# Kernel optimization log

Measured on AMD Instinct MI355X. Metric: run time of the kernel, lower is better.

## Reference

```python
import jax, jax.numpy as jnp
import numpy as np

B, N, DIM = 4, 2048, 1024
HEADS, DIM_HEAD = 16, 64
INNER = HEADS * DIM_HEAD  # 1024
SCALE = DIM_HEAD ** -0.5


def setup_inputs() -> dict:
    key = jax.random.key(0)
    k_x, k_qkv, k_out, k_b = jax.random.split(key, 4)
    x = jax.random.normal(k_x, (B, N, DIM), dtype=jnp.float32)
    # nn.Linear weights, stored transposed for x @ W convenience
    w_qkv = jax.random.normal(k_qkv, (DIM, 3 * INNER), dtype=jnp.float32) * (DIM ** -0.5)
    w_out = jax.random.normal(k_out, (INNER, DIM), dtype=jnp.float32) * (INNER ** -0.5)
    b_out = jax.random.normal(k_b, (DIM,), dtype=jnp.float32) * 0.01
    return {"x": x, "w_qkv": w_qkv, "w_out": w_out, "b_out": b_out}


def _split_heads(t):
    # 'b n (h d) -> (b h) n d'
    b, n, _ = t.shape
    return t.reshape(b, n, HEADS, DIM_HEAD).transpose(0, 2, 1, 3).reshape(b * HEADS, n, DIM_HEAD)


def reference(x, w_qkv, w_out, b_out):
    b, n, _ = x.shape
    qkv = x @ w_qkv  # [b, n, 3*inner]
    q, k, v = jnp.split(qkv, 3, axis=-1)
    q = q * SCALE
    q, k, v = map(_split_heads, (q, k, v))  # [(b h), n, d]
    sim = jnp.einsum('bid,bjd->bij', q, k)  # [(b h), n, n]
    a = jax.nn.softmax(sim, axis=-1)
    out = jnp.einsum('bij,bjd->bid', a, v)  # [(b h), n, d]
    # '(b h) n d -> b n (h d)'
    out = out.reshape(b, HEADS, n, DIM_HEAD).transpose(0, 2, 1, 3).reshape(b, n, INNER)
    return out @ w_out + b_out  # dropout p=0.0 is identity
```

## Files before the change

### kernel.cpp

```cpp
#include <hip/hip_runtime.h>
#include <stdint.h>


typedef uint16_t u16;
typedef __bf16 bf16x8 __attribute__((ext_vector_type(8)));
typedef float f32x4 __attribute__((ext_vector_type(4)));
typedef unsigned u32x2 __attribute__((ext_vector_type(2)));
typedef unsigned u32x4 __attribute__((ext_vector_type(4)));

#define AS3(p) ((__attribute__((address_space(3))) uint32_t*)(p))
#define AS1(p) ((const __attribute__((address_space(1))) uint32_t*)(p))

__device__ __forceinline__ void gl_lds16(const void* g, void* lds) {
  __builtin_amdgcn_global_load_lds(AS1(g), AS3(lds), 16, 0, 0);
}

__device__ __forceinline__ u16 f2bf(float f) {
  union { __bf16 b; u16 u; } x; x.b = (__bf16)f;
  return x.u;
}

__global__ void cvt_f32_bf16(const float* __restrict__ in, u16* __restrict__ out, long n) {
  long i = ((long)blockIdx.x * 256 + threadIdx.x) * 8;
  if (i >= n) return;
  u16 r[8];
  #pragma unroll
  for (int j = 0; j < 8; ++j) r[j] = f2bf(in[i + j]);
  *(uint4*)(out + i) = *(const uint4*)r;
}

__global__ void transpose2_f2b(const float* __restrict__ in0, u16* __restrict__ out0,
                               const float* __restrict__ in1, u16* __restrict__ out1,
                               int C0, int C1) {
  const int R = 1024;
  const float* in = blockIdx.z ? in1 : in0;
  u16* out = blockIdx.z ? out1 : out0;
  int C = blockIdx.z ? C1 : C0;
  int c0 = blockIdx.x * 32;
  if (c0 >= C) return;
  __shared__ u16 tile[32][33];
  int tx = threadIdx.x, ty = threadIdx.y;
  int r0 = blockIdx.y * 32;
  #pragma unroll
  for (int i = 0; i < 4; ++i)
    tile[ty + 8 * i][tx] = f2bf(in[(long)(r0 + ty + 8 * i) * C + c0 + tx]);
  __syncthreads();
  #pragma unroll
  for (int i = 0; i < 4; ++i)
    out[(long)(c0 + ty + 8 * i) * R + r0 + tx] = tile[tx][ty + 8 * i];
}

template <bool BIAS, bool OUTF32>
__global__ __launch_bounds__(256) void gemm_bt(const u16* __restrict__ A, const u16* __restrict__ Bt,
                                               const float* __restrict__ bias, void* __restrict__ Cv,
                                               int M, int N, int K, int qcols, float qscale) {
  __shared__ u16 smem[32768];
  const int tid = threadIdx.x;
  const int w = tid >> 6, l = tid & 63;
  const int l15 = l & 15, lh = l >> 4;
  const int wr = w >> 1, wc = w & 1;
  int bid = blockIdx.x + blockIdx.y * gridDim.x;
  int xcd = bid & 7, idx = bid >> 3;
  int by = xcd * (gridDim.y >> 3) + idx / gridDim.x;
  int bx = idx % gridDim.x;
  const long row0 = (long)by * 128, col0 = (long)bx * 128;

  const f32x4 fzero = {0.f, 0.f, 0.f, 0.f};
  f32x4 acc[4][4];
  #pragma unroll
  for (int m = 0; m < 4; ++m)
    #pragma unroll
    for (int n = 0; n < 4; ++n) acc[m][n] = fzero;

  const int nkt = K >> 6;
  #pragma unroll
  for (int i = 0; i < 4; ++i) {
    int c = w * 256 + i * 64 + l;
    int row = c >> 3, sub = c & 7;
    int col8 = (sub ^ (row & 7)) * 8;
    gl_lds16(A + (row0 + row) * K + col8, (void*)(smem + w * 2048 + i * 512));
    gl_lds16(Bt + (col0 + row) * K + col8, (void*)(smem + 8192 + w * 2048 + i * 512));
  }
  __syncthreads();

  for (int t = 0; t < nkt; ++t) {
    const int curA = (t & 1) ? 16384 : 0;
    const int curB = (t & 1) ? 24576 : 8192;
    const int nxtA = (t & 1) ? 0 : 16384;
    const int nxtB = (t & 1) ? 8192 : 24576;

    if (t + 1 < nkt) {
      const int kt = (t + 1) << 6;
      #pragma unroll
      for (int i = 0; i < 4; ++i) {
        int c = w * 256 + i * 64 + l;
        int row = c >> 3, sub = c & 7;
        int col8 = (sub ^ (row & 7)) * 8;
        gl_lds16(A + (row0 + row) * K + kt + col8, (void*)(smem + nxtA + w * 2048 + i * 512));
        gl_lds16(Bt + (col0 + row) * K + kt + col8, (void*)(smem + nxtB + w * 2048 + i * 512));
      }
    }

    #pragma unroll
    for (int ks = 0; ks < 2; ++ks) {
      bf16x8 a[4], b[4];
      #pragma unroll
      for (int m = 0; m < 4; ++m) {
        int row = wr * 64 + m * 16 + l15;
        a[m] = *(const bf16x8*)&smem[curA + row * 64 + ((ks * 32 + lh * 8) ^ ((row & 7) << 3))];
      }
      #pragma unroll
      for (int n = 0; n < 4; ++n) {
        int row = wc * 64 + n * 16 + l15;
        b[n] = *(const bf16x8*)&smem[curB + row * 64 + ((ks * 32 + lh * 8) ^ ((row & 7) << 3))];
      }
      __builtin_amdgcn_s_setprio(1);
      #pragma unroll
      for (int m = 0; m < 4; ++m)
        #pragma unroll
        for (int n = 0; n < 4; ++n)
          acc[m][n] = __builtin_amdgcn_mfma_f32_16x16x32_bf16(a[m], b[n], acc[m][n], 0, 0, 0);
      __builtin_amdgcn_s_setprio(0);
    }

    __syncthreads();
  }

  #pragma unroll
  for (int n = 0; n < 4; ++n) {
    long col = col0 + wc * 64 + n * 16 + l15;
    float bv = 0.f;
    if (BIAS) bv = bias[col];
    float scl = (col < qcols) ? qscale : 1.0f;
    #pragma unroll
    for (int m = 0; m < 4; ++m) {
      #pragma unroll
      for (int r = 0; r < 4; ++r) {
        long row = row0 + wr * 64 + m * 16 + lh * 4 + r;
        if (OUTF32) ((float*)Cv)[row * N + col] = acc[m][n][r] + bv;
        else        ((u16*)Cv)[row * N + col] = f2bf(acc[m][n][r] * scl + bv);
      }
    }
  }
}

__global__ __launch_bounds__(512, 4) void attn_k(const u16* __restrict__ qkv, u16* __restrict__ attn) {
  __shared__ u16 smem[24576];
  const int tid = threadIdx.x;
  const int w = tid >> 6, l = tid & 63;
  const int l15 = l & 15, lh = l >> 4;
  const int b = blockIdx.x >> 4, h = blockIdx.x & 15;
  const int qt = blockIdx.y;
  const long rs = 3072;
  const long qrow0 = (long)b * 2048 + qt * 256;
  const u16* Qg    = qkv + qrow0 * rs + h * 64;
  const u16* Kbase = qkv + (long)b * 2048 * rs + 1024 + h * 64;
  const u16* Vbase = qkv + (long)b * 2048 * rs + 2048 + h * 64;

  #pragma unroll
  for (int i = 0; i < 4; ++i) {
    int c = (w * 4 + i) * 64 + l;
    int row = c >> 3;
    int col8 = ((c & 7) ^ (row & 7)) * 8;
    gl_lds16(Qg + (long)row * rs + col8, (void*)(smem + (w * 4 + i) * 512));
  }
  {
    int c = tid;
    int row = c >> 3;
    int col8 = ((c & 7) ^ (row & 7)) * 8;
    gl_lds16(Kbase + (long)row * rs + col8, (void*)(smem + 16384 + w * 512));

    int kv0 = (tid & 31) * 2, d0 = (tid >> 5) * 4;
    const u16* Vg = Vbase + (long)kv0 * rs + d0;
    u32x2 va = *(const u32x2*)Vg;
    u32x2 vb = *(const u32x2*)(Vg + rs);
    const u16* pa = (const u16*)&va;
    const u16* pb = (const u16*)&vb;
    #pragma unroll
    for (int jj = 0; jj < 4; ++jj) {
      int d = d0 + jj;
      *(uint32_t*)&smem[20480 + d * 64 + (kv0 ^ ((d & 7) << 3))] =
          (uint32_t)pa[jj] | ((uint32_t)pb[jj] << 16);
    }
  }
  __syncthreads();

  bf16x8 aq[2][2];
  #pragma unroll
  for (int m = 0; m < 2; ++m)
    #pragma unroll
    for (int ks = 0; ks < 2; ++ks) {
      int row = w * 32 + m * 16 + l15;
      aq[m][ks] = *(const bf16x8*)&smem[row * 64 + ((ks * 32 + lh * 8) ^ ((row & 7) << 3))];
    }
  __syncthreads();

  bf16x8 ones;
  { union { u32x4 u; bf16x8 f; } cv; cv.u = (u32x4){0x3F803F80u, 0x3F803F80u, 0x3F803F80u, 0x3F803F80u}; ones = cv.f; }

  const f32x4 fzero = {0.f, 0.f, 0.f, 0.f};
  f32x4 acc[2][4];
  f32x4 acc_l[2];
  #pragma unroll
  for (int m = 0; m < 2; ++m) {
    acc_l[m] = fzero;
    #pragma unroll
    for (int n = 0; n < 4; ++n) acc[m][n] = fzero;
  }

  for (int t = 0; t < 32; ++t) {
    const int kOff  = (t & 1) ? 0     : 16384;
    const int vOff  = (t & 1) ? 4096  : 20480;
    const int kOffN = (t & 1) ? 16384 : 0;
    const int vOffN = (t & 1) ? 20480 : 4096;

    f32x4 s[2][4];
    #pragma unroll
    for (int m = 0; m < 2; ++m)
      #pragma unroll
      for (int n = 0; n < 4; ++n) s[m][n] = fzero;
    #pragma unroll
    for (int ks = 0; ks < 2; ++ks) {
      bf16x8 bk[4];
      #pragma unroll
      for (int n = 0; n < 4; ++n) {
        int row = n * 16 + l15;
        bk[n] = *(const bf16x8*)&smem[kOff + row * 64 + ((ks * 32 + lh * 8) ^ ((row & 7) << 3))];
      }
      __builtin_amdgcn_s_setprio(1);
      #pragma unroll
      for (int m = 0; m < 2; ++m)
        #pragma unroll
        for (int n = 0; n < 4; ++n)
          s[m][n] = __builtin_amdgcn_mfma_f32_16x16x32_bf16(bk[n], aq[m][ks], s[m][n], 0, 0, 0);
      __builtin_amdgcn_s_setprio(0);
    }

    uint4 kreg;
    u32x2 va, vb;
    int kv0 = (tid & 31) * 2, d0v = (tid >> 5) * 4;
    if (t < 31) {
      int row = tid >> 3, sub = tid & 7;
      kreg = *(const uint4*)(Kbase + ((long)(t + 1) * 64 + row) * rs + sub * 8);
      const u16* Vg = Vbase + ((long)(t + 1) * 64 + kv0) * rs + d0v;
      va = *(const u32x2*)Vg;
      vb = *(const u32x2*)(Vg + rs);
    }

    unsigned Wm[2][4][2];
    #pragma unroll
    for (int m = 0; m < 2; ++m) {
      #pragma unroll
      for (int n = 0; n < 4; ++n) {
        float p0 = __builtin_amdgcn_exp2f(s[m][n][0]);
        float p1 = __builtin_amdgcn_exp2f(s[m][n][1]);
        float p2 = __builtin_amdgcn_exp2f(s[m][n][2]);
        float p3 = __builtin_amdgcn_exp2f(s[m][n][3]);
        Wm[m][n][0] = (unsigned)f2bf(p0) | ((unsigned)f2bf(p1) << 16);
        Wm[m][n][1] = (unsigned)f2bf(p2) | ((unsigned)f2bf(p3) << 16);
      }
    }

    #pragma unroll
    for (int ks = 0; ks < 2; ++ks) {
      bf16x8 pf[2];
      #pragma unroll
      for (int m = 0; m < 2; ++m) {
        unsigned a0 = Wm[m][2 * ks][0], b0 = Wm[m][2 * ks + 1][0];
        unsigned a1 = Wm[m][2 * ks][1], b1 = Wm[m][2 * ks + 1][1];
        asm("v_permlane32_swap_b32 %0, %1" : "+v"(a0), "+v"(b0));
        asm("v_permlane16_swap_b32 %0, %1" : "+v"(a0), "+v"(b0));
        asm("v_permlane32_swap_b32 %0, %1" : "+v"(a1), "+v"(b1));
        asm("v_permlane16_swap_b32 %0, %1" : "+v"(a1), "+v"(b1));
        union { u32x4 u; bf16x8 f; } cv;
        cv.u = (u32x4){a0, a1, b0, b1};
        pf[m] = cv.f;
      }
      bf16x8 bv4[4];
      #pragma unroll
      for (int n = 0; n < 4; ++n) {
        int vr = n * 16 + l15;
        bv4[n] = *(const bf16x8*)&smem[vOff + vr * 64 + ((ks * 32 + lh * 8) ^ ((vr & 7) << 3))];
      }
      __builtin_amdgcn_s_setprio(1);
      #pragma unroll
      for (int n = 0; n < 4; ++n)
        #pragma unroll
        for (int m = 0; m < 2; ++m)
          acc[m][n] = __builtin_amdgcn_mfma_f32_16x16x32_bf16(bv4[n], pf[m], acc[m][n], 0, 0, 0);
      #pragma unroll
      for (int m = 0; m < 2; ++m)
        acc_l[m] = __builtin_amdgcn_mfma_f32_16x16x32_bf16(ones, pf[m], acc_l[m], 0, 0, 0);
      __builtin_amdgcn_s_setprio(0);
    }

    if (t < 31) {
      int row = tid >> 3, sub = tid & 7;
      *(uint4*)&smem[kOffN + row * 64 + (sub ^ (row & 7)) * 8] = kreg;
      const u16* pa = (const u16*)&va;
      const u16* pb = (const u16*)&vb;
      #pragma unroll
      for (int jj = 0; jj < 4; ++jj) {
        int d = d0v + jj;
        *(uint32_t*)&smem[vOffN + d * 64 + (kv0 ^ ((d & 7) << 3))] =
            (uint32_t)pa[jj] | ((uint32_t)pb[jj] << 16);
      }
      __syncthreads();
    }
  }

  #pragma unroll
  for (int m = 0; m < 2; ++m) {
    float inv = 1.0f / acc_l[m][0];
    long q = qrow0 + w * 32 + m * 16 + l15;
    #pragma unroll
    for (int n = 0; n < 4; ++n) {
      unsigned lo = (unsigned)f2bf(acc[m][n][0] * inv) | ((unsigned)f2bf(acc[m][n][1] * inv) << 16);
      unsigned hi = (unsigned)f2bf(acc[m][n][2] * inv) | ((unsigned)f2bf(acc[m][n][3] * inv) << 16);
      *(u32x2*)&attn[q * 1024 + h * 64 + n * 16 + lh * 4] = (u32x2){lo, hi};
    }
  }
}

extern "C" void kernel_launch(void* const* d_in, const int* in_sizes, int n_in,
                              void* d_out, int out_size, void* d_ws, size_t ws_size,
                              hipStream_t stream) {
  (void)in_sizes; (void)n_in; (void)out_size; (void)ws_size;
  const float* x     = (const float*)d_in[0];
  const float* w_qkv = (const float*)d_in[1];
  const float* w_out = (const float*)d_in[2];
  const float* b_out = (const float*)d_in[3];
  float* out = (float*)d_out;

  u16* ws    = (u16*)d_ws;
  u16* wqkvT = ws;
  u16* woutT = wqkvT + (size_t)3072 * 1024;
  u16* xbf   = woutT + (size_t)1024 * 1024;
  u16* qkv   = xbf   + (size_t)8192 * 1024;
  u16* attnb = qkv   + (size_t)8192 * 3072;

  const float QSCALE = 0.125f * 1.44269504088896f;

  cvt_f32_bf16<<<4096, 256, 0, stream>>>(x, xbf, (long)8192 * 1024);
  transpose2_f2b<<<dim3(96, 32, 2), dim3(32, 8), 0, stream>>>(w_qkv, wqkvT, w_out, woutT, 3072, 1024);
  gemm_bt<false, false><<<dim3(24, 64), 256, 0, stream>>>(xbf, wqkvT, nullptr, qkv,
                                                          8192, 3072, 1024, 1024, QSCALE);
  attn_k<<<dim3(64, 8), 512, 0, stream>>>(qkv, attnb);
  gemm_bt<true, true><<<dim3(8, 64), 256, 0, stream>>>(attnb, woutT, b_out, out,
                                                       8192, 1024, 1024, 0, 1.0f);
}
```

Measured before the change: 181.8 us.

## Halve attention query tile to 128 rows and double grid size

The attention kernel now handles 128 query rows per block instead of 256, with one 16-row query fragment per wave, and launches twice as many blocks. Q is loaded straight from global memory into registers instead of being staged through LDS, so LDS per block drops to 32KB and the occupancy hint rises to 6. The aim is more blocks across the CUs and more resident waves. The cost is that each K/V tile is loaded and transposed twice as often per query row, and each K/V LDS read feeds half as many MFMAs.

```diff
diff --git a/kernel.cpp b/kernel.cpp
--- a/kernel.cpp
+++ b/kernel.cpp
@@ -144,31 +144,27 @@
   }
 }
 
-__global__ __launch_bounds__(512, 4) void attn_k(const u16* __restrict__ qkv, u16* __restrict__ attn) {
-  __shared__ u16 smem[24576];
+__global__ __launch_bounds__(512, 6) void attn_k(const u16* __restrict__ qkv, u16* __restrict__ attn) {
+  __shared__ u16 smem[16384];
   const int tid = threadIdx.x;
   const int w = tid >> 6, l = tid & 63;
   const int l15 = l & 15, lh = l >> 4;
   const int b = blockIdx.x >> 4, h = blockIdx.x & 15;
   const int qt = blockIdx.y;
   const long rs = 3072;
-  const long qrow0 = (long)b * 2048 + qt * 256;
-  const u16* Qg    = qkv + qrow0 * rs + h * 64;
+  const long qrow0 = (long)b * 2048 + qt * 128;
   const u16* Kbase = qkv + (long)b * 2048 * rs + 1024 + h * 64;
   const u16* Vbase = qkv + (long)b * 2048 * rs + 2048 + h * 64;
 
-  #pragma unroll
-  for (int i = 0; i < 4; ++i) {
-    int c = (w * 4 + i) * 64 + l;
-    int row = c >> 3;
-    int col8 = ((c & 7) ^ (row & 7)) * 8;
-    gl_lds16(Qg + (long)row * rs + col8, (void*)(smem + (w * 4 + i) * 512));
-  }
+  bf16x8 aq[2];
+  #pragma unroll
+  for (int ks = 0; ks < 2; ++ks)
+    aq[ks] = *(const bf16x8*)(qkv + (qrow0 + w * 16 + l15) * rs + h * 64 + ks * 32 + lh * 8);
+
   {
-    int c = tid;
-    int row = c >> 3;
-    int col8 = ((c & 7) ^ (row & 7)) * 8;
-    gl_lds16(Kbase + (long)row * rs + col8, (void*)(smem + 16384 + w * 512));
+    int row = tid >> 3, sub = tid & 7;
+    int col8 = (sub ^ (row & 7)) * 8;
+    gl_lds16(Kbase + (long)row * rs + col8, (void*)(smem + w * 512));
 
     int kv0 = (tid & 31) * 2, d0 = (tid >> 5) * 4;
     const u16* Vg = Vbase + (long)kv0 * rs + d0;
@@ -179,46 +175,31 @@
     #pragma unroll
     for (int jj = 0; jj < 4; ++jj) {
       int d = d0 + jj;
-      *(uint32_t*)&smem[20480 + d * 64 + (kv0 ^ ((d & 7) << 3))] =
+      *(uint32_t*)&smem[4096 + d * 64 + (kv0 ^ ((d & 7) << 3))] =
           (uint32_t)pa[jj] | ((uint32_t)pb[jj] << 16);
     }
   }
-  __syncthreads();
-
-  bf16x8 aq[2][2];
-  #pragma unroll
-  for (int m = 0; m < 2; ++m)
-    #pragma unroll
-    for (int ks = 0; ks < 2; ++ks) {
-      int row = w * 32 + m * 16 + l15;
-      aq[m][ks] = *(const bf16x8*)&smem[row * 64 + ((ks * 32 + lh * 8) ^ ((row & 7) << 3))];
-    }
   __syncthreads();
 
   bf16x8 ones;
   { union { u32x4 u; bf16x8 f; } cv; cv.u = (u32x4){0x3F803F80u, 0x3F803F80u, 0x3F803F80u, 0x3F803F80u}; ones = cv.f; }
 
   const f32x4 fzero = {0.f, 0.f, 0.f, 0.f};
-  f32x4 acc[2][4];
-  f32x4 acc_l[2];
-  #pragma unroll
-  for (int m = 0; m < 2; ++m) {
-    acc_l[m] = fzero;
-    #pragma unroll
-    for (int n = 0; n < 4; ++n) acc[m][n] = fzero;
-  }
+  f32x4 acc[4];
+  f32x4 acc_l;
+  acc_l = fzero;
+  #pragma unroll
+  for (int n = 0; n < 4; ++n) acc[n] = fzero;
 
   for (int t = 0; t < 32; ++t) {
-    const int kOff  = (t & 1) ? 0     : 16384;
-    const int vOff  = (t & 1) ? 4096  : 20480;
-    const int kOffN = (t & 1) ? 16384 : 0;
-    const int vOffN = (t & 1) ? 20480 : 4096;
-
-    f32x4 s[2][4];
-    #pragma unroll
-    for (int m = 0; m < 2; ++m)
-      #pragma unroll
-      for (int n = 0; n < 4; ++n) s[m][n] = fzero;
+    const int kOff  = (t & 1) ? 8192  : 0;
+    const int vOff  = (t & 1) ? 12288 : 4096;
+    const int kOffN = (t & 1) ? 0     : 8192;
+    const int vOffN = (t & 1) ? 4096  : 12288;
+
+    f32x4 s[4];
+    #pragma unroll
+    for (int n = 0; n < 4; ++n) s[n] = fzero;
     #pragma unroll
     for (int ks = 0; ks < 2; ++ks) {
       bf16x8 bk[4];
@@ -229,10 +210,8 @@
       }
       __builtin_amdgcn_s_setprio(1);
       #pragma unroll
-      for (int m = 0; m < 2; ++m)
-        #pragma unroll
-        for (int n = 0; n < 4; ++n)
-          s[m][n] = __builtin_amdgcn_mfma_f32_16x16x32_bf16(bk[n], aq[m][ks], s[m][n], 0, 0, 0);
+      for (int n = 0; n < 4; ++n)
+        s[n] = __builtin_amdgcn_mfma_f32_16x16x32_bf16(bk[n], aq[ks], s[n], 0, 0, 0);
       __builtin_amdgcn_s_setprio(0);
     }
 
@@ -247,35 +226,28 @@
       vb = *(const u32x2*)(Vg + rs);
     }
 
-    unsigned Wm[2][4][2];
-    #pragma unroll
-    for (int m = 0; m < 2; ++m) {
-      #pragma unroll
-      for (int n = 0; n < 4; ++n) {
-        float p0 = __builtin_amdgcn_exp2f(s[m][n][0]);
-        float p1 = __builtin_amdgcn_exp2f(s[m][n][1]);
-        float p2 = __builtin_amdgcn_exp2f(s[m][n][2]);
-        float p3 = __builtin_amdgcn_exp2f(s[m][n][3]);
-        Wm[m][n][0] = (unsigned)f2bf(p0) | ((unsigned)f2bf(p1) << 16);
-        Wm[m][n][1] = (unsigned)f2bf(p2) | ((unsigned)f2bf(p3) << 16);
-      }
+    unsigned Wm[4][2];
+    #pragma unroll
+    for (int n = 0; n < 4; ++n) {
+      float p0 = __builtin_amdgcn_exp2f(s[n][0]);
+      float p1 = __builtin_amdgcn_exp2f(s[n][1]);
+      float p2 = __builtin_amdgcn_exp2f(s[n][2]);
+      float p3 = __builtin_amdgcn_exp2f(s[n][3]);
+      Wm[n][0] = (unsigned)f2bf(p0) | ((unsigned)f2bf(p1) << 16);
+      Wm[n][1] = (unsigned)f2bf(p2) | ((unsigned)f2bf(p3) << 16);
     }
 
     #pragma unroll
     for (int ks = 0; ks < 2; ++ks) {
-      bf16x8 pf[2];
-      #pragma unroll
-      for (int m = 0; m < 2; ++m) {
-        unsigned a0 = Wm[m][2 * ks][0], b0 = Wm[m][2 * ks + 1][0];
-        unsigned a1 = Wm[m][2 * ks][1], b1 = Wm[m][2 * ks + 1][1];
-        asm("v_permlane32_swap_b32 %0, %1" : "+v"(a0), "+v"(b0));
-        asm("v_permlane16_swap_b32 %0, %1" : "+v"(a0), "+v"(b0));
-        asm("v_permlane32_swap_b32 %0, %1" : "+v"(a1), "+v"(b1));
-        asm("v_permlane16_swap_b32 %0, %1" : "+v"(a1), "+v"(b1));
-        union { u32x4 u; bf16x8 f; } cv;
-        cv.u = (u32x4){a0, a1, b0, b1};
-        pf[m] = cv.f;
-      }
+      unsigned a0 = Wm[2 * ks][0], b0 = Wm[2 * ks + 1][0];
+      unsigned a1 = Wm[2 * ks][1], b1 = Wm[2 * ks + 1][1];
+      asm("v_permlane32_swap_b32 %0, %1" : "+v"(a0), "+v"(b0));
+      asm("v_permlane16_swap_b32 %0, %1" : "+v"(a0), "+v"(b0));
+      asm("v_permlane32_swap_b32 %0, %1" : "+v"(a1), "+v"(b1));
+      asm("v_permlane16_swap_b32 %0, %1" : "+v"(a1), "+v"(b1));
+      union { u32x4 u; bf16x8 f; } cv;
+      cv.u = (u32x4){a0, a1, b0, b1};
+      bf16x8 pf = cv.f;
       bf16x8 bv4[4];
       #pragma unroll
       for (int n = 0; n < 4; ++n) {
@@ -285,12 +257,8 @@
       __builtin_amdgcn_s_setprio(1);
       #pragma unroll
       for (int n = 0; n < 4; ++n)
-        #pragma unroll
-        for (int m = 0; m < 2; ++m)
-          acc[m][n] = __builtin_amdgcn_mfma_f32_16x16x32_bf16(bv4[n], pf[m], acc[m][n], 0, 0, 0);
-      #pragma unroll
-      for (int m = 0; m < 2; ++m)
-        acc_l[m] = __builtin_amdgcn_mfma_f32_16x16x32_bf16(ones, pf[m], acc_l[m], 0, 0, 0);
+        acc[n] = __builtin_amdgcn_mfma_f32_16x16x32_bf16(bv4[n], pf, acc[n], 0, 0, 0);
+      acc_l = __builtin_amdgcn_mfma_f32_16x16x32_bf16(ones, pf, acc_l, 0, 0, 0);
       __builtin_amdgcn_s_setprio(0);
     }
 
@@ -309,14 +277,13 @@
     }
   }
 
-  #pragma unroll
-  for (int m = 0; m < 2; ++m) {
-    float inv = 1.0f / acc_l[m][0];
-    long q = qrow0 + w * 32 + m * 16 + l15;
+  {
+    float inv = 1.0f / acc_l[0];
+    long q = qrow0 + w * 16 + l15;
     #pragma unroll
     for (int n = 0; n < 4; ++n) {
-      unsigned lo = (unsigned)f2bf(acc[m][n][0] * inv) | ((unsigned)f2bf(acc[m][n][1] * inv) << 16);
-      unsigned hi = (unsigned)f2bf(acc[m][n][2] * inv) | ((unsigned)f2bf(acc[m][n][3] * inv) << 16);
+      unsigned lo = (unsigned)f2bf(acc[n][0] * inv) | ((unsigned)f2bf(acc[n][1] * inv) << 16);
+      unsigned hi = (unsigned)f2bf(acc[n][2] * inv) | ((unsigned)f2bf(acc[n][3] * inv) << 16);
       *(u32x2*)&attn[q * 1024 + h * 64 + n * 16 + lh * 4] = (u32x2){lo, hi};
     }
   }
@@ -345,7 +312,7 @@
   transpose2_f2b<<<dim3(96, 32, 2), dim3(32, 8), 0, stream>>>(w_qkv, wqkvT, w_out, woutT, 3072, 1024);
   gemm_bt<false, false><<<dim3(24, 64), 256, 0, stream>>>(xbf, wqkvT, nullptr, qkv,
                                                           8192, 3072, 1024, 1024, QSCALE);
-  attn_k<<<dim3(64, 8), 512, 0, stream>>>(qkv, attnb);
+  attn_k<<<dim3(64, 16), 512, 0, stream>>>(qkv, attnb);
   gemm_bt<true, true><<<dim3(8, 64), 256, 0, stream>>>(attnb, woutT, b_out, out,
                                                        8192, 1024, 1024, 0, 1.0f);
 }
```

New measurement: 205.9 us. 1.13x slower.

## Fuse fp32-to-bf16 conversion of x into QKV GEMM A-tile loads

Applied to the files above, without the earlier changes.

Removes the separate conversion kernel and the intermediate bf16 copy of x. The QKV GEMM now loads fp32 A tiles into registers, converts them to bf16, and stores them to LDS after the MFMA step, in place of asynchronous global-to-LDS loads. This saves one launch and one full round trip of x through memory. The cost is more register pressure, doubled A-tile bytes across repeated column blocks, and loss of the direct-to-LDS load path.

```diff
diff --git a/kernel.cpp b/kernel.cpp
--- a/kernel.cpp
+++ b/kernel.cpp
@@ -20,13 +20,13 @@
   return x.u;
 }
 
-__global__ void cvt_f32_bf16(const float* __restrict__ in, u16* __restrict__ out, long n) {
-  long i = ((long)blockIdx.x * 256 + threadIdx.x) * 8;
-  if (i >= n) return;
-  u16 r[8];
-  #pragma unroll
-  for (int j = 0; j < 8; ++j) r[j] = f2bf(in[i + j]);
-  *(uint4*)(out + i) = *(const uint4*)r;
+__device__ __forceinline__ uint4 pack8(const float4 a, const float4 b) {
+  uint4 r;
+  r.x = (unsigned)f2bf(a.x) | ((unsigned)f2bf(a.y) << 16);
+  r.y = (unsigned)f2bf(a.z) | ((unsigned)f2bf(a.w) << 16);
+  r.z = (unsigned)f2bf(b.x) | ((unsigned)f2bf(b.y) << 16);
+  r.w = (unsigned)f2bf(b.z) | ((unsigned)f2bf(b.w) << 16);
+  return r;
 }
 
 __global__ void transpose2_f2b(const float* __restrict__ in0, u16* __restrict__ out0,
@@ -50,8 +50,8 @@
     out[(long)(c0 + ty + 8 * i) * R + r0 + tx] = tile[tx][ty + 8 * i];
 }
 
-template <bool BIAS, bool OUTF32>
-__global__ __launch_bounds__(256) void gemm_bt(const u16* __restrict__ A, const u16* __restrict__ Bt,
+template <bool AF32, bool BIAS, bool OUTF32>
+__global__ __launch_bounds__(256) void gemm_bt(const void* __restrict__ Av, const u16* __restrict__ Bt,
                                                const float* __restrict__ bias, void* __restrict__ Cv,
                                                int M, int N, int K, int qcols, float qscale) {
   __shared__ u16 smem[32768];
@@ -65,6 +65,9 @@
   int bx = idx % gridDim.x;
   const long row0 = (long)by * 128, col0 = (long)bx * 128;
 
+  const u16* Ab = (const u16*)Av;
+  const float* Af = (const float*)Av;
+
   const f32x4 fzero = {0.f, 0.f, 0.f, 0.f};
   f32x4 acc[4][4];
   #pragma unroll
@@ -78,7 +81,12 @@
     int c = w * 256 + i * 64 + l;
     int row = c >> 3, sub = c & 7;
     int col8 = (sub ^ (row & 7)) * 8;
-    gl_lds16(A + (row0 + row) * K + col8, (void*)(smem + w * 2048 + i * 512));
+    if constexpr (AF32) {
+      const float* src = Af + (row0 + row) * K + col8;
+      *(uint4*)&smem[(unsigned)c * 8] = pack8(*(const float4*)src, *(const float4*)(src + 4));
+    } else {
+      gl_lds16(Ab + (row0 + row) * K + col8, (void*)(smem + w * 2048 + i * 512));
+    }
     gl_lds16(Bt + (col0 + row) * K + col8, (void*)(smem + 8192 + w * 2048 + i * 512));
   }
   __syncthreads();
@@ -89,6 +97,7 @@
     const int nxtA = (t & 1) ? 0 : 16384;
     const int nxtB = (t & 1) ? 8192 : 24576;
 
+    float4 fa[4][2];
     if (t + 1 < nkt) {
       const int kt = (t + 1) << 6;
       #pragma unroll
@@ -96,7 +105,13 @@
         int c = w * 256 + i * 64 + l;
         int row = c >> 3, sub = c & 7;
         int col8 = (sub ^ (row & 7)) * 8;
-        gl_lds16(A + (row0 + row) * K + kt + col8, (void*)(smem + nxtA + w * 2048 + i * 512));
+        if constexpr (AF32) {
+          const float* src = Af + (row0 + row) * K + kt + col8;
+          fa[i][0] = *(const float4*)src;
+          fa[i][1] = *(const float4*)(src + 4);
+        } else {
+          gl_lds16(Ab + (row0 + row) * K + kt + col8, (void*)(smem + nxtA + w * 2048 + i * 512));
+        }
         gl_lds16(Bt + (col0 + row) * K + kt + col8, (void*)(smem + nxtB + w * 2048 + i * 512));
       }
     }
@@ -121,6 +136,16 @@
         for (int n = 0; n < 4; ++n)
           acc[m][n] = __builtin_amdgcn_mfma_f32_16x16x32_bf16(a[m], b[n], acc[m][n], 0, 0, 0);
       __builtin_amdgcn_s_setprio(0);
+    }
+
+    if (t + 1 < nkt) {
+      if constexpr (AF32) {
+        #pragma unroll
+        for (int i = 0; i < 4; ++i) {
+          int c = w * 256 + i * 64 + l;
+          *(uint4*)&smem[nxtA + (unsigned)c * 8] = pack8(fa[i][0], fa[i][1]);
+        }
+      }
     }
 
     __syncthreads();
@@ -335,17 +360,15 @@
   u16* ws    = (u16*)d_ws;
   u16* wqkvT = ws;
   u16* woutT = wqkvT + (size_t)3072 * 1024;
-  u16* xbf   = woutT + (size_t)1024 * 1024;
-  u16* qkv   = xbf   + (size_t)8192 * 1024;
+  u16* qkv   = woutT + (size_t)1024 * 1024;
   u16* attnb = qkv   + (size_t)8192 * 3072;
 
   const float QSCALE = 0.125f * 1.44269504088896f;
 
-  cvt_f32_bf16<<<4096, 256, 0, stream>>>(x, xbf, (long)8192 * 1024);
   transpose2_f2b<<<dim3(96, 32, 2), dim3(32, 8), 0, stream>>>(w_qkv, wqkvT, w_out, woutT, 3072, 1024);
-  gemm_bt<false, false><<<dim3(24, 64), 256, 0, stream>>>(xbf, wqkvT, nullptr, qkv,
-                                                          8192, 3072, 1024, 1024, QSCALE);
+  gemm_bt<true, false, false><<<dim3(24, 64), 256, 0, stream>>>(x, wqkvT, nullptr, qkv,
+                                                                8192, 3072, 1024, 1024, QSCALE);
   attn_k<<<dim3(64, 8), 512, 0, stream>>>(qkv, attnb);
-  gemm_bt<true, true><<<dim3(8, 64), 256, 0, stream>>>(attnb, woutT, b_out, out,
-                                                       8192, 1024, 1024, 0, 1.0f);
-}
+  gemm_bt<false, true, true><<<dim3(8, 64), 256, 0, stream>>>(attnb, woutT, b_out, out,
+                                                              8192, 1024, 1024, 0, 1.0f);
+}
```

After: 205.3 us. 12.9% more time.
